# Kernel optimization log

Hardware: AMD Instinct MI355X
Metric: run time of the kernel (lower is better)

Reference implementation:

```python
import jax, jax.numpy as jnp
import numpy as np

B = 262144
L, C, H, W = 256, 3, 256, 256


def setup_inputs() -> dict:
    key = jax.random.key(0)
    k1, k2, k3 = jax.random.split(key, 3)
    X = jax.random.normal(k1, (B, 4), dtype=jnp.float32)
    light_shots = jax.random.normal(k2, (L, C, H, W), dtype=jnp.float32)
    light_positions = jax.random.normal(k3, (L, 2), dtype=jnp.float32)
    return {"X": X, "light_shots": light_shots, "light_positions": light_positions}


def _barycentric(corners, points):
    # corners: [B, 3, 2], points: [B, 2]
    v0 = corners[:, 1] - corners[:, 0]
    v1 = corners[:, 2] - corners[:, 0]
    v2 = points - corners[:, 0]
    d00 = (v0 * v0).sum(1)
    d11 = (v1 * v1).sum(1)
    d01 = (v0 * v1).sum(1)
    d20 = (v2 * v0).sum(1)
    d21 = (v2 * v1).sum(1)
    denom = d00 * d11 - d01 * d01
    v = (d11 * d20 - d01 * d21) / denom
    w = (d00 * d21 - d01 * d20) / denom
    u = 1.0 - v - w
    uvw = jnp.stack([u, v, w], axis=1)
    outside = ((uvw < 0) | jnp.isnan(uvw)).any(axis=1)
    t = jnp.clip(d20 / d00, 0.0, 1.0)
    fallback = jnp.stack([1.0 - t, t, jnp.zeros_like(t)], axis=1)
    return jnp.where(outside[:, None], fallback, uvw)


def _grid_sample_3d_border(vol, pts):
    # vol: [C, D, Hh, Ww]; pts: [N, 3] with normalized (x->W, y->H, z->D)
    # align_corners=True, padding_mode='border', trilinear.
    Cc, D, Hh, Ww = vol.shape

    def unnorm(c, size):
        return jnp.clip((c + 1.0) * 0.5 * (size - 1), 0.0, size - 1.0)

    px = unnorm(pts[:, 0], Ww)
    py = unnorm(pts[:, 1], Hh)
    pz = unnorm(pts[:, 2], D)
    x0 = jnp.floor(px).astype(jnp.int32)
    y0 = jnp.floor(py).astype(jnp.int32)
    z0 = jnp.floor(pz).astype(jnp.int32)
    x1 = jnp.minimum(x0 + 1, Ww - 1)
    y1 = jnp.minimum(y0 + 1, Hh - 1)
    z1 = jnp.minimum(z0 + 1, D - 1)
    wx = px - x0
    wy = py - y0
    wz = pz - z0

    def g(zi, yi, xi):
        return vol[:, zi, yi, xi]  # [C, N]

    out = (
        g(z0, y0, x0) * ((1 - wz) * (1 - wy) * (1 - wx))
        + g(z0, y0, x1) * ((1 - wz) * (1 - wy) * wx)
        + g(z0, y1, x0) * ((1 - wz) * wy * (1 - wx))
        + g(z0, y1, x1) * ((1 - wz) * wy * wx)
        + g(z1, y0, x0) * (wz * (1 - wy) * (1 - wx))
        + g(z1, y0, x1) * (wz * (1 - wy) * wx)
        + g(z1, y1, x0) * (wz * wy * (1 - wx))
        + g(z1, y1, x1) * (wz * wy * wx)
    )
    return out.T  # [N, C]


def reference(X, light_shots, light_positions):
    n_lights = light_positions.shape[0]
    # top-3 nearest lights in direction space (cols 2:4)
    d2 = ((X[:, None, 2:] - light_positions[None]) ** 2).sum(axis=2)  # [B, L]
    _, light_ind = jax.lax.top_k(-d2, 3)  # ascending distance, sorted
    light_corners = light_positions[light_ind]  # [B, 3, 2]
    light_weights = _barycentric(light_corners, X[:, 2:])  # [B, 3]
    xy = jnp.repeat(X[:, :2], 3, axis=0)  # [3B, 2]
    z = light_ind.reshape(-1).astype(X.dtype) / ((n_lights - 1) / 2) - 1.0
    pts = jnp.column_stack([xy, z])  # [3B, 3]
    vol = jnp.transpose(light_shots, (1, 0, 2, 3))  # [3, L, H, W]
    light_colors = _grid_sample_3d_border(vol, pts).reshape(-1, 3, 3)  # [B, 3, 3]
    return (light_weights[:, :, None] * light_colors).sum(axis=1)  # [B, 3]
```

## Files before the change

kernel.cpp:

```cpp
#include <hip/hip_runtime.h>

constexpr int NL = 256;
constexpr int HW = 256;

struct __attribute__((aligned(4))) F2 { float a, b; };

__global__ __launch_bounds__(256)
void lsf_kernel(const float* __restrict__ X,
                const float* __restrict__ shots,
                const float* __restrict__ lpos,
                float* __restrict__ out, int B)
{
    __shared__ float2 s_lp[NL];
    for (int i = threadIdx.x; i < NL; i += 256)
        s_lp[i] = reinterpret_cast<const float2*>(lpos)[i];
    __syncthreads();

    int b = blockIdx.x * 256 + threadIdx.x;
    if (b >= B) return;

    float4 xv = reinterpret_cast<const float4*>(X)[b];
    float qx = xv.z, qy = xv.w;

    float dd0 = INFINITY, dd1 = INFINITY, dd2 = INFINITY;
    int i0 = 0, i1 = 0, i2 = 0;
    #pragma unroll 4
    for (int i = 0; i < NL; ++i) {
        float2 lp = s_lp[i];
        float dx = qx - lp.x, dy = qy - lp.y;
        float d = dx * dx + dy * dy;
        bool c0 = d < dd0, c1 = d < dd1, c2 = d < dd2;
        dd2 = c1 ? dd1 : (c2 ? d : dd2);
        i2  = c1 ? i1  : (c2 ? i : i2);
        dd1 = c0 ? dd0 : (c1 ? d : dd1);
        i1  = c0 ? i0  : (c1 ? i : i1);
        dd0 = c0 ? d   : dd0;
        i0  = c0 ? i   : i0;
    }

    float2 p0 = s_lp[i0], p1 = s_lp[i1], p2c = s_lp[i2];
    float v0x = p1.x - p0.x,  v0y = p1.y - p0.y;
    float v1x = p2c.x - p0.x, v1y = p2c.y - p0.y;
    float v2x = qx - p0.x,    v2y = qy - p0.y;
    float d00 = v0x * v0x + v0y * v0y;
    float d11 = v1x * v1x + v1y * v1y;
    float d01 = v0x * v1x + v0y * v1y;
    float d20 = v2x * v0x + v2y * v0y;
    float d21 = v2x * v1x + v2y * v1y;
    float denom = d00 * d11 - d01 * d01;
    float v = (d11 * d20 - d01 * d21) / denom;
    float w = (d00 * d21 - d01 * d20) / denom;
    float u = 1.0f - v - w;
    bool inside = (u >= 0.f) & (v >= 0.f) & (w >= 0.f);
    float t = fminf(fmaxf(d20 / d00, 0.f), 1.f);
    float w0 = inside ? u : (1.f - t);
    float w1 = inside ? v : t;
    float w2 = inside ? w : 0.f;

    float px = fminf(fmaxf((xv.x + 1.f) * 0.5f * (HW - 1), 0.f), (float)(HW - 1));
    float py = fminf(fmaxf((xv.y + 1.f) * 0.5f * (HW - 1), 0.f), (float)(HW - 1));
    int x0 = (int)floorf(px), y0 = (int)floorf(py);
    int y1 = min(y0 + 1, HW - 1);
    float wx = px - (float)x0, wy = py - (float)y0;
    float w00 = (1.f - wy) * (1.f - wx), w01 = (1.f - wy) * wx;
    float w10 = wy * (1.f - wx),         w11 = wy * wx;
    int  xe  = min(x0, HW - 2);
    bool xhi = (x0 == HW - 1);

    int idx3[3] = { i0, i1, i2 };
    F2 G0[9], G1[9];
    #pragma unroll
    for (int k = 0; k < 3; ++k) {
        const float* base = shots + (size_t)idx3[k] * (3 * HW * HW);
        #pragma unroll
        for (int c = 0; c < 3; ++c) {
            const float* p = base + c * (HW * HW) + xe;
            int j = k * 3 + c;
            G0[j] = *reinterpret_cast<const F2*>(p + y0 * HW);
            G1[j] = *reinterpret_cast<const F2*>(p + y1 * HW);
        }
    }
    __builtin_amdgcn_sched_barrier(0);

    float wk3[3] = { w0, w1, w2 };
    float acc[3] = { 0.f, 0.f, 0.f };
    #pragma unroll
    for (int k = 0; k < 3; ++k) {
        #pragma unroll
        for (int c = 0; c < 3; ++c) {
            int j = k * 3 + c;
            float v00 = xhi ? G0[j].b : G0[j].a;
            float v10 = xhi ? G1[j].b : G1[j].a;
            acc[c] += wk3[k] * (v00 * w00 + G0[j].b * w01 +
                                v10 * w10 + G1[j].b * w11);
        }
    }

    out[(size_t)b * 3 + 0] = acc[0];
    out[(size_t)b * 3 + 1] = acc[1];
    out[(size_t)b * 3 + 2] = acc[2];
}

extern "C" void kernel_launch(void* const* d_in, const int* in_sizes, int n_in,
                              void* d_out, int out_size, void* d_ws, size_t ws_size,
                              hipStream_t stream) {
    const float* X     = (const float*)d_in[0];
    const float* shots = (const float*)d_in[1];
    const float* lpos  = (const float*)d_in[2];
    float* out = (float*)d_out;
    int B = in_sizes[0] / 4;
    int grid = (B + 255) / 256;
    lsf_kernel<<<grid, 256, 0, stream>>>(X, shots, lpos, out, B);
}
```

Before: 88.72 us.

## Split each query across two lanes for top-3 search and bilinear rows

Each query point is now handled by two adjacent lanes. Each lane scans half of the 256 lights for its top-3, and the two partial lists are merged through lane shuffles. Each lane then fetches one of the two bilinear rows and the partial sums are combined by shuffle, which halves the serial work and gather registers per thread while doubling the thread count. It also adds a launch_bounds occupancy hint and 32-bit offset arithmetic for the gathers. The cost is extra shuffles, duplicated barycentric work in both lanes, and tie-breaking order that could differ from the sequential scan.

Measured after the change: 84.55 us. -4.7%, faster.

```diff
diff --git a/kernel.cpp b/kernel.cpp
--- a/kernel.cpp
+++ b/kernel.cpp
@@ -5,7 +5,7 @@
 
 struct __attribute__((aligned(4))) F2 { float a, b; };
 
-__global__ __launch_bounds__(256)
+__global__ __launch_bounds__(256, 8)
 void lsf_kernel(const float* __restrict__ X,
                 const float* __restrict__ shots,
                 const float* __restrict__ lpos,
@@ -16,27 +16,43 @@
         s_lp[i] = reinterpret_cast<const float2*>(lpos)[i];
     __syncthreads();
 
-    int b = blockIdx.x * 256 + threadIdx.x;
-    if (b >= B) return;
+    int tid = blockIdx.x * 256 + threadIdx.x;
+    int p   = tid >> 1;
+    int h   = tid & 1;
+    if (p >= B) return;
 
-    float4 xv = reinterpret_cast<const float4*>(X)[b];
+    float4 xv = reinterpret_cast<const float4*>(X)[p];
     float qx = xv.z, qy = xv.w;
 
     float dd0 = INFINITY, dd1 = INFINITY, dd2 = INFINITY;
     int i0 = 0, i1 = 0, i2 = 0;
+    auto visit = [&](float d, int idx) {
+        bool c0 = d < dd0, c1 = d < dd1, c2 = d < dd2;
+        dd2 = c1 ? dd1 : (c2 ? d : dd2);
+        i2  = c1 ? i1  : (c2 ? idx : i2);
+        dd1 = c0 ? dd0 : (c1 ? d : dd1);
+        i1  = c0 ? i0  : (c1 ? idx : i1);
+        dd0 = c0 ? d   : dd0;
+        i0  = c0 ? idx : i0;
+    };
+    int base = h * (NL / 2);
     #pragma unroll 4
-    for (int i = 0; i < NL; ++i) {
+    for (int i = base; i < base + NL / 2; ++i) {
         float2 lp = s_lp[i];
         float dx = qx - lp.x, dy = qy - lp.y;
-        float d = dx * dx + dy * dy;
-        bool c0 = d < dd0, c1 = d < dd1, c2 = d < dd2;
-        dd2 = c1 ? dd1 : (c2 ? d : dd2);
-        i2  = c1 ? i1  : (c2 ? i : i2);
-        dd1 = c0 ? dd0 : (c1 ? d : dd1);
-        i1  = c0 ? i0  : (c1 ? i : i1);
-        dd0 = c0 ? d   : dd0;
-        i0  = c0 ? i   : i0;
+        visit(dx * dx + dy * dy, i);
     }
+
+    float ad0 = __shfl_xor(dd0, 1), ad1 = __shfl_xor(dd1, 1), ad2 = __shfl_xor(dd2, 1);
+    int   ai0 = __shfl_xor(i0, 1),  ai1 = __shfl_xor(i1, 1),  ai2 = __shfl_xor(i2, 1);
+    float hd0 = h ? dd0 : ad0, hd1 = h ? dd1 : ad1, hd2 = h ? dd2 : ad2;
+    int   hi0 = h ? i0  : ai0, hi1 = h ? i1  : ai1, hi2 = h ? i2  : ai2;
+    float ld0 = h ? ad0 : dd0, ld1 = h ? ad1 : dd1, ld2 = h ? ad2 : dd2;
+    int   li0 = h ? ai0 : i0,  li1 = h ? ai1 : i1,  li2 = h ? ai2 : i2;
+    dd0 = ld0; dd1 = ld1; dd2 = ld2; i0 = li0; i1 = li1; i2 = li2;
+    visit(hd0, hi0);
+    visit(hd1, hi1);
+    visit(hd2, hi2);
 
     float2 p0 = s_lp[i0], p1 = s_lp[i1], p2c = s_lp[i2];
     float v0x = p1.x - p0.x,  v0y = p1.y - p0.y;
@@ -62,43 +78,45 @@
     int x0 = (int)floorf(px), y0 = (int)floorf(py);
     int y1 = min(y0 + 1, HW - 1);
     float wx = px - (float)x0, wy = py - (float)y0;
-    float w00 = (1.f - wy) * (1.f - wx), w01 = (1.f - wy) * wx;
-    float w10 = wy * (1.f - wx),         w11 = wy * wx;
     int  xe  = min(x0, HW - 2);
     bool xhi = (x0 == HW - 1);
+    int   row = h ? y1 : y0;
+    float rw  = h ? wy : (1.f - wy);
 
     int idx3[3] = { i0, i1, i2 };
-    F2 G0[9], G1[9];
+    F2 G[9];
     #pragma unroll
     for (int k = 0; k < 3; ++k) {
-        const float* base = shots + (size_t)idx3[k] * (3 * HW * HW);
+        unsigned lo = (unsigned)(idx3[k] * 3) << 16;
         #pragma unroll
         for (int c = 0; c < 3; ++c) {
-            const float* p = base + c * (HW * HW) + xe;
-            int j = k * 3 + c;
-            G0[j] = *reinterpret_cast<const F2*>(p + y0 * HW);
-            G1[j] = *reinterpret_cast<const F2*>(p + y1 * HW);
+            unsigned off = lo + ((unsigned)c << 16) + (unsigned)(row * HW + xe);
+            G[k * 3 + c] = *reinterpret_cast<const F2*>(shots + off);
         }
     }
     __builtin_amdgcn_sched_barrier(0);
 
     float wk3[3] = { w0, w1, w2 };
-    float acc[3] = { 0.f, 0.f, 0.f };
+    float s0 = 0.f, s1 = 0.f, s2 = 0.f;
     #pragma unroll
     for (int k = 0; k < 3; ++k) {
-        #pragma unroll
-        for (int c = 0; c < 3; ++c) {
-            int j = k * 3 + c;
-            float v00 = xhi ? G0[j].b : G0[j].a;
-            float v10 = xhi ? G1[j].b : G1[j].a;
-            acc[c] += wk3[k] * (v00 * w00 + G0[j].b * w01 +
-                                v10 * w10 + G1[j].b * w11);
-        }
+        float r0 = (xhi ? G[k*3+0].b : G[k*3+0].a) * (1.f - wx) + G[k*3+0].b * wx;
+        float r1 = (xhi ? G[k*3+1].b : G[k*3+1].a) * (1.f - wx) + G[k*3+1].b * wx;
+        float r2 = (xhi ? G[k*3+2].b : G[k*3+2].a) * (1.f - wx) + G[k*3+2].b * wx;
+        s0 += wk3[k] * r0;
+        s1 += wk3[k] * r1;
+        s2 += wk3[k] * r2;
     }
+    s0 *= rw; s1 *= rw; s2 *= rw;
 
-    out[(size_t)b * 3 + 0] = acc[0];
-    out[(size_t)b * 3 + 1] = acc[1];
-    out[(size_t)b * 3 + 2] = acc[2];
+    float t0 = s0 + __shfl_xor(s0, 1);
+    float t1 = s1 + __shfl_xor(s1, 1);
+    float t2 = s2 + __shfl_xor(s2, 1);
+    if (h == 0) {
+        out[(size_t)p * 3 + 0] = t0;
+        out[(size_t)p * 3 + 1] = t1;
+        out[(size_t)p * 3 + 2] = t2;
+    }
 }
 
 extern "C" void kernel_launch(void* const* d_in, const int* in_sizes, int n_in,
@@ -109,6 +127,7 @@
     const float* lpos  = (const float*)d_in[2];
     float* out = (float*)d_out;
     int B = in_sizes[0] / 4;
-    int grid = (B + 255) / 256;
+    long long T = 2LL * B;
+    int grid = (int)((T + 255) / 256);
     lsf_kernel<<<grid, 256, 0, stream>>>(X, shots, lpos, out, B);
 }
```
